# Optimization experiments

Measured on AMD Instinct MI355X. Metric: run time of the kernel, lower is better.

## Reference

```python
import jax, jax.numpy as jnp
import numpy as np

N_NODES = 50000
N_EDGES = 800000
D = 128
NEG_SLOPE = 0.2
L2_EPS = 1e-12  # torch F.normalize eps


def setup_inputs() -> dict:
    key = jax.random.key(0)
    k1, k2, k3, k4, k5 = jax.random.split(key, 5)
    node_fts = jax.random.normal(k1, (N_NODES, D), dtype=jnp.float32)
    edges = jax.random.randint(k2, (2, N_EDGES), 0, N_NODES, dtype=jnp.int32)
    edge_fts = jax.random.normal(k3, (N_EDGES, 1), dtype=jnp.float32)
    # xavier-ish init for linear weights (stored as [out, in], matching nn.Linear)
    scale = 1.414 * np.sqrt(2.0 / (D + D))
    W_self = jax.random.normal(k4, (D, D), dtype=jnp.float32) * scale
    W_neigh = jax.random.normal(k5, (D, D), dtype=jnp.float32) * scale
    return {"node_fts": node_fts, "edges": edges, "edge_fts": edge_fts,
            "W_self": W_self, "W_neigh": W_neigh}


def reference(node_fts, edges, edge_fts, W_self, W_neigh):
    n = node_fts.shape[0]
    dst_idx = edges[0]  # segment ids (aggregation targets)
    src_idx = edges[1]  # gather ids (neighbor features)

    # self transform: [N, D]
    src_node_fts = node_fts @ W_self.T

    # gather neighbor feats along edges: [E, D]
    gathered = node_fts[src_idx]

    # scatter-mean into destination nodes
    seg_sum = jax.ops.segment_sum(gathered, dst_idx, num_segments=n)  # [N, D]
    cnt = jax.ops.segment_sum(jnp.ones((gathered.shape[0], 1), dtype=node_fts.dtype),
                              dst_idx, num_segments=n)                # [N, 1]
    neigh_mean = seg_sum / jnp.maximum(cnt, 1.0)

    # linear + LeakyReLU(0.2) on aggregated neighbors
    neigh_final = jax.nn.leaky_relu(neigh_mean @ W_neigh.T, NEG_SLOPE)

    # update: sum + LeakyReLU(0.2)
    updated = jax.nn.leaky_relu(src_node_fts + neigh_final, NEG_SLOPE)

    # L2 normalize per row (torch F.normalize semantics)
    norm = jnp.linalg.norm(updated, axis=1, keepdims=True)
    return updated / jnp.maximum(norm, L2_EPS)
```

## Files before the change

### kernel.cpp

```cpp
#include <hip/hip_runtime.h>
#include <hip/hip_bf16.h>

#define N_NODES 50000
#define N_EDGES 800000
#define D 128
#define NEG 0.2f

#define NB 200
#define EPB 4000
#define NPAIR 12500
#define NCH 8
#define ROWS_PER_CH 25

#define MFMA_BLOCKS 782
#define COLA_BLOCKS 391
#define FILL_SLICES 1600
#define FILL_EPS 500

typedef __attribute__((ext_vector_type(8))) short bf16x8;
typedef __attribute__((ext_vector_type(4))) float f32x4;

__device__ __forceinline__ float bflo(unsigned int u) {
    return __uint_as_float(u << 16);
}
__device__ __forceinline__ float bfhi(unsigned int u) {
    return __uint_as_float(u & 0xffff0000u);
}

__global__ __launch_bounds__(256) void hist_convert_kernel(
    const int* __restrict__ dst_idx,
    unsigned int* __restrict__ bh,
    unsigned char* __restrict__ rank8,
    const float4* __restrict__ ws4, const float4* __restrict__ wn4,
    ushort4* __restrict__ wb4) {
    __shared__ unsigned int lh[NPAIR];
    const int tid = threadIdx.x, b = blockIdx.x;
    if (b < NB) {
        for (int i = tid; i < NPAIR; i += 256) lh[i] = 0u;
        __syncthreads();
        const int e0 = b * EPB;
        for (int i = tid; i < EPB; i += 256) {
            int d = dst_idx[e0 + i];
            int sh = (d & 3) * 8;
            unsigned int old = atomicAdd(&lh[d >> 2], 1u << sh);
            rank8[e0 + i] = (unsigned char)((old >> sh) & 0xffu);
        }
        __syncthreads();
        for (int i = tid; i < NPAIR; i += 256) bh[(size_t)b * NPAIR + i] = lh[i];
    } else {
        int i = (b - NB) * 256 + tid;
        const int NW = D * D / 4;
        if (i < 2 * NW) {
            float4 v = (i < NW) ? ws4[i] : wn4[i - NW];
            ushort4 o;
            __hip_bfloat16 h;
            h = __float2bfloat16(v.x); o.x = reinterpret_cast<unsigned short&>(h);
            h = __float2bfloat16(v.y); o.y = reinterpret_cast<unsigned short&>(h);
            h = __float2bfloat16(v.z); o.z = reinterpret_cast<unsigned short&>(h);
            h = __float2bfloat16(v.w); o.w = reinterpret_cast<unsigned short&>(h);
            wb4[i] = o;
        }
    }
}

__global__ __launch_bounds__(256) void mfma_colA_kernel(
    const float* __restrict__ x, const ushort* __restrict__ wb,
    unsigned int* __restrict__ sb32, unsigned int* __restrict__ zb32,
    const unsigned int* __restrict__ bh, unsigned int* __restrict__ csum) {
    __shared__ ushort tile[4][2][16][132];
    if (blockIdx.x < MFMA_BLOCKS) {
        const int lane = threadIdx.x & 63;
        const int wv = threadIdx.x >> 6;
        const int wglobal = blockIdx.x * 4 + wv;
        if (wglobal >= N_NODES / 16) return;
        const int m0 = wglobal * 16;
        const int lm = lane & 15;
        const int lk = (lane >> 4) * 8;

        bf16x8 a[4];
#pragma unroll
        for (int kc = 0; kc < 4; ++kc) {
            const float* src = x + (long)(m0 + lm) * D + kc * 32 + lk;
            float4 f0 = *(const float4*)(src);
            float4 f1 = *(const float4*)(src + 4);
            bf16x8 af;
            __hip_bfloat16 h;
            h = __float2bfloat16(f0.x); af[0] = reinterpret_cast<short&>(h);
            h = __float2bfloat16(f0.y); af[1] = reinterpret_cast<short&>(h);
            h = __float2bfloat16(f0.z); af[2] = reinterpret_cast<short&>(h);
            h = __float2bfloat16(f0.w); af[3] = reinterpret_cast<short&>(h);
            h = __float2bfloat16(f1.x); af[4] = reinterpret_cast<short&>(h);
            h = __float2bfloat16(f1.y); af[5] = reinterpret_cast<short&>(h);
            h = __float2bfloat16(f1.z); af[6] = reinterpret_cast<short&>(h);
            h = __float2bfloat16(f1.w); af[7] = reinterpret_cast<short&>(h);
            a[kc] = af;
        }

        const int dr = (lane >> 4) * 4;
        ushort (*ts)[132] = tile[wv][0];
        ushort (*tz)[132] = tile[wv][1];
#pragma unroll
        for (int nt = 0; nt < 16; ++nt) {
            f32x4 acc = {0.f, 0.f, 0.f, 0.f};
#pragma unroll
            for (int kc = 0; kc < 4; ++kc) {
                bf16x8 bfr = *(const bf16x8*)(wb + (nt * 16 + lm) * D + kc * 32 + lk);
                acc = __builtin_amdgcn_mfma_f32_16x16x32_bf16(a[kc], bfr, acc, 0, 0, 0);
            }
            ushort (*t)[132] = (nt < 8) ? ts : tz;
            const int col = (nt & 7) * 16 + lm;
#pragma unroll
            for (int r = 0; r < 4; ++r) {
                __hip_bfloat16 h = __float2bfloat16(acc[r]);
                t[dr + r][col] = reinterpret_cast<unsigned short&>(h);
            }
        }
        const unsigned int* ts32 = (const unsigned int*)ts;
        const unsigned int* tz32 = (const unsigned int*)tz;
#pragma unroll
        for (int r16 = 0; r16 < 16; ++r16) {
            sb32[(m0 + r16) * 64 + lane] = ts32[r16 * 66 + lane];
            zb32[(m0 + r16) * 64 + lane] = tz32[r16 * 66 + lane];
        }
    } else {
        int gid = (blockIdx.x - MFMA_BLOCKS) * 256 + threadIdx.x;
        if (gid >= NCH * NPAIR) return;
        int c = gid / NPAIR;
        int i = gid - c * NPAIR;
        const unsigned int* col = bh + (size_t)(c * ROWS_PER_CH) * NPAIR + i;
        unsigned int s = 0u;
#pragma unroll
        for (int r = 0; r < ROWS_PER_CH; ++r) s += col[(size_t)r * NPAIR];
        csum[c * NPAIR + i] = s;
    }
}

__global__ __launch_bounds__(1024) void colscanb_scan_kernel(
    unsigned int* __restrict__ bh, const unsigned int* __restrict__ csum,
    int* __restrict__ offs) {
    const int tid = threadIdx.x;
    if (blockIdx.x < 98) {
        int gid = blockIdx.x * 1024 + tid;
        if (gid >= NCH * NPAIR) return;
        int c = gid / NPAIR;
        int i = gid - c * NPAIR;
        unsigned int run = 0u;
        for (int cc = 0; cc < c; ++cc) run += csum[cc * NPAIR + i];
        unsigned int* col = bh + (size_t)(c * ROWS_PER_CH) * NPAIR + i;
#pragma unroll
        for (int r = 0; r < ROWS_PER_CH; ++r) {
            unsigned int v = col[(size_t)r * NPAIR];
            col[(size_t)r * NPAIR] = run;
            run += v;
        }
        return;
    }
    __shared__ int wsum[16];
    __shared__ int carry_s;
    const int lane = tid & 63, wv = tid >> 6;
    if (tid == 0) { carry_s = 0; offs[N_NODES] = N_EDGES; }
    __syncthreads();
    for (int base = 0; base < NPAIR; base += 4096) {
        int i0 = base + tid * 4;
        unsigned int p0 = 0, p1 = 0, p2 = 0, p3 = 0;
#pragma unroll
        for (int j = 0; j < 4; ++j) {
            int qi = i0 + j;
            if (qi < NPAIR) {
                unsigned int s = 0;
#pragma unroll
                for (int c = 0; c < NCH; ++c) s += csum[c * NPAIR + qi];
                if (j == 0) p0 = s; else if (j == 1) p1 = s;
                else if (j == 2) p2 = s; else p3 = s;
            }
        }
        int q0 = (int)((p0 & 0xffu) + ((p0 >> 8) & 0xffu) + ((p0 >> 16) & 0xffu) + (p0 >> 24));
        int q1 = (int)((p1 & 0xffu) + ((p1 >> 8) & 0xffu) + ((p1 >> 16) & 0xffu) + (p1 >> 24));
        int q2 = (int)((p2 & 0xffu) + ((p2 >> 8) & 0xffu) + ((p2 >> 16) & 0xffu) + (p2 >> 24));
        int q3 = (int)((p3 & 0xffu) + ((p3 >> 8) & 0xffu) + ((p3 >> 16) & 0xffu) + (p3 >> 24));
        int tsum = q0 + q1 + q2 + q3;
        int xs = tsum;
#pragma unroll
        for (int off = 1; off < 64; off <<= 1) {
            int y = __shfl_up(xs, off);
            if (lane >= off) xs += y;
        }
        if (lane == 63) wsum[wv] = xs;
        __syncthreads();
        if (wv == 0 && lane < 16) {
            int s = wsum[lane];
#pragma unroll
            for (int off = 1; off < 16; off <<= 1) {
                int y = __shfl_up(s, off);
                if (lane >= off) s += y;
            }
            wsum[lane] = s;
        }
        __syncthreads();
        int waveoff = (wv == 0) ? 0 : wsum[wv - 1];
        int excl = carry_s + waveoff + xs - tsum;
        unsigned int pk[4] = {p0, p1, p2, p3};
        int qs[4] = {q0, q1, q2, q3};
        int qbase = excl;
#pragma unroll
        for (int j = 0; j < 4; ++j) {
            int qi = i0 + j;
            if (qi < NPAIR) {
                unsigned int p = pk[j];
                int d0 = (int)(p & 0xffu), d1 = (int)((p >> 8) & 0xffu);
                int d2 = (int)((p >> 16) & 0xffu);
                int4 o; o.x = qbase; o.y = o.x + d0; o.z = o.y + d1; o.w = o.z + d2;
                *(int4*)(offs + 4 * qi) = o;
            }
            qbase += qs[j];
        }
        int total = wsum[15];
        __syncthreads();
        if (tid == 0) carry_s += total;
        __syncthreads();
    }
}

__global__ __launch_bounds__(256) void fill_kernel(
    const int* __restrict__ dst_idx, const int* __restrict__ src_idx,
    const unsigned char* __restrict__ rank8,
    const unsigned char* __restrict__ bprefix,
    const int* __restrict__ offs, unsigned short* __restrict__ adj) {
    const int e0 = blockIdx.x * FILL_EPS;
    const int b = e0 / EPB;
    const unsigned char* bp = bprefix + (size_t)b * N_NODES;
    for (int i = threadIdx.x; i < FILL_EPS; i += 256) {
        int e = e0 + i;
        int d = dst_idx[e];
        int pos = offs[d] + (int)bp[d] + (int)rank8[e];
        adj[pos] = (unsigned short)src_idx[e];
    }
}

__global__ __launch_bounds__(256) void gather_final_kernel(
    const uint4* __restrict__ zb4, const uint4* __restrict__ sb4,
    const int* __restrict__ offs,
    const unsigned short* __restrict__ adj, float4* __restrict__ out4) {
    int wid = (int)((blockIdx.x * (long)blockDim.x + threadIdx.x) >> 6);
    int lane = threadIdx.x & 63;
    if (wid >= N_NODES) return;
    const int c = lane & 15, g = lane >> 4;
    int base = offs[wid];
    int len = offs[wid + 1] - base;

    float a0 = 0.f, a1 = 0.f, a2 = 0.f, a3 = 0.f;
    float a4 = 0.f, a5 = 0.f, a6 = 0.f, a7 = 0.f;

    int k = 0;
    for (; k + 8 <= len; k += 8) {
        unsigned int sA = adj[base + k + g];
        unsigned int sB = adj[base + k + 4 + g];
        uint4 vA = zb4[sA * 16u + c];
        uint4 vB = zb4[sB * 16u + c];
        a0 += bflo(vA.x); a1 += bfhi(vA.x);
        a2 += bflo(vA.y); a3 += bfhi(vA.y);
        a4 += bflo(vA.z); a5 += bfhi(vA.z);
        a6 += bflo(vA.w); a7 += bfhi(vA.w);
        a0 += bflo(vB.x); a1 += bfhi(vB.x);
        a2 += bflo(vB.y); a3 += bfhi(vB.y);
        a4 += bflo(vB.z); a5 += bfhi(vB.z);
        a6 += bflo(vB.w); a7 += bfhi(vB.w);
    }
    if (k + 4 <= len) {
        unsigned int sA = adj[base + k + g];
        uint4 vA = zb4[sA * 16u + c];
        a0 += bflo(vA.x); a1 += bfhi(vA.x);
        a2 += bflo(vA.y); a3 += bfhi(vA.y);
        a4 += bflo(vA.z); a5 += bfhi(vA.z);
        a6 += bflo(vA.w); a7 += bfhi(vA.w);
        k += 4;
    }
    int rem = len - k;
    if (g < rem) {
        unsigned int sA = adj[base + k + g];
        uint4 vA = zb4[sA * 16u + c];
        a0 += bflo(vA.x); a1 += bfhi(vA.x);
        a2 += bflo(vA.y); a3 += bfhi(vA.y);
        a4 += bflo(vA.z); a5 += bfhi(vA.z);
        a6 += bflo(vA.w); a7 += bfhi(vA.w);
    }

    a0 += __shfl_xor(a0, 16); a1 += __shfl_xor(a1, 16);
    a2 += __shfl_xor(a2, 16); a3 += __shfl_xor(a3, 16);
    a4 += __shfl_xor(a4, 16); a5 += __shfl_xor(a5, 16);
    a6 += __shfl_xor(a6, 16); a7 += __shfl_xor(a7, 16);
    a0 += __shfl_xor(a0, 32); a1 += __shfl_xor(a1, 32);
    a2 += __shfl_xor(a2, 32); a3 += __shfl_xor(a3, 32);
    a4 += __shfl_xor(a4, 32); a5 += __shfl_xor(a5, 32);
    a6 += __shfl_xor(a6, 32); a7 += __shfl_xor(a7, 32);

    float inv = 1.0f / fmaxf((float)len, 1.0f);
    float m0 = a0 * inv, m1 = a1 * inv, m2 = a2 * inv, m3 = a3 * inv;
    float m4 = a4 * inv, m5 = a5 * inv, m6 = a6 * inv, m7 = a7 * inv;
    m0 = m0 > 0.f ? m0 : NEG * m0; m1 = m1 > 0.f ? m1 : NEG * m1;
    m2 = m2 > 0.f ? m2 : NEG * m2; m3 = m3 > 0.f ? m3 : NEG * m3;
    m4 = m4 > 0.f ? m4 : NEG * m4; m5 = m5 > 0.f ? m5 : NEG * m5;
    m6 = m6 > 0.f ? m6 : NEG * m6; m7 = m7 > 0.f ? m7 : NEG * m7;

    uint4 sv = sb4[(unsigned int)wid * 16u + c];
    float u0 = bflo(sv.x) + m0, u1 = bfhi(sv.x) + m1;
    float u2 = bflo(sv.y) + m2, u3 = bfhi(sv.y) + m3;
    float u4 = bflo(sv.z) + m4, u5 = bfhi(sv.z) + m5;
    float u6 = bflo(sv.w) + m6, u7 = bfhi(sv.w) + m7;
    u0 = u0 > 0.f ? u0 : NEG * u0; u1 = u1 > 0.f ? u1 : NEG * u1;
    u2 = u2 > 0.f ? u2 : NEG * u2; u3 = u3 > 0.f ? u3 : NEG * u3;
    u4 = u4 > 0.f ? u4 : NEG * u4; u5 = u5 > 0.f ? u5 : NEG * u5;
    u6 = u6 > 0.f ? u6 : NEG * u6; u7 = u7 > 0.f ? u7 : NEG * u7;

    float ss = u0 * u0 + u1 * u1 + u2 * u2 + u3 * u3 +
               u4 * u4 + u5 * u5 + u6 * u6 + u7 * u7;
    ss += __shfl_xor(ss, 1);
    ss += __shfl_xor(ss, 2);
    ss += __shfl_xor(ss, 4);
    ss += __shfl_xor(ss, 8);
    float r = 1.0f / fmaxf(sqrtf(ss), 1e-12f);

    if (lane < 16) {
        float4 o0; o0.x = u0 * r; o0.y = u1 * r; o0.z = u2 * r; o0.w = u3 * r;
        float4 o1; o1.x = u4 * r; o1.y = u5 * r; o1.z = u6 * r; o1.w = u7 * r;
        out4[(unsigned int)wid * 32u + c * 2u] = o0;
        out4[(unsigned int)wid * 32u + c * 2u + 1u] = o1;
    }
}

extern "C" void kernel_launch(void* const* d_in, const int* in_sizes, int n_in,
                              void* d_out, int out_size, void* d_ws, size_t ws_size,
                              hipStream_t stream) {
    const float* node_fts = (const float*)d_in[0];
    const int* edges = (const int*)d_in[1];
    const float* W_self = (const float*)d_in[3];
    const float* W_neigh = (const float*)d_in[4];

    const int* dst_idx = edges;
    const int* src_idx = edges + N_EDGES;

    unsigned short* zb = (unsigned short*)d_ws;
    unsigned short* sb = zb + (size_t)N_NODES * D;
    unsigned short* wb = sb + (size_t)N_NODES * D;
    int* offs = (int*)(wb + 256 * 128);
    unsigned short* adj = (unsigned short*)(offs + N_NODES + 1);
    unsigned int* bh = (unsigned int*)(adj + N_EDGES);
    unsigned char* rank8 = (unsigned char*)(bh + (size_t)NB * NPAIR);
    unsigned int* csum = (unsigned int*)(rank8 + N_EDGES);

    hist_convert_kernel<<<NB + 32, 256, 0, stream>>>(
        dst_idx, bh, rank8,
        (const float4*)W_self, (const float4*)W_neigh, (ushort4*)wb);

    mfma_colA_kernel<<<MFMA_BLOCKS + COLA_BLOCKS, 256, 0, stream>>>(
        node_fts, wb, (unsigned int*)sb, (unsigned int*)zb, bh, csum);

    colscanb_scan_kernel<<<99, 1024, 0, stream>>>(bh, csum, offs);

    fill_kernel<<<FILL_SLICES, 256, 0, stream>>>(
        dst_idx, src_idx, rank8, (const unsigned char*)bh, offs, adj);

    int gb = (N_NODES * 64 + 255) / 256;
    gather_final_kernel<<<gb, 256, 0, stream>>>(
        (const uint4*)zb, (const uint4*)sb, offs, adj, (float4*)d_out);
}
```

Baseline: 122.3 us.

## Replace per-block histogram CSR build with global atomic count and atomic fill

Replaces the blocked byte-packed histogram, column sums and two-level scan with a global atomic count per destination node, a single-block scan fused into the MFMA kernel, and an atomic cursor in the fill kernel. This drops one kernel launch plus the large bh/csum traffic, but adds a memset and global atomics on 50k counters. Edge order within each adjacency list is no longer deterministic, so floating-point summation order can vary between runs. The single scan block now runs serially over 50k entries alongside the MFMA blocks.

```diff
diff --git a/kernel.cpp b/kernel.cpp
--- a/kernel.cpp
+++ b/kernel.cpp
@@ -6,16 +6,11 @@
 #define D 128
 #define NEG 0.2f
 
-#define NB 200
-#define EPB 4000
-#define NPAIR 12500
-#define NCH 8
-#define ROWS_PER_CH 25
-
+#define CNT_BLOCKS 800
+#define CNT_EPB 1000
 #define MFMA_BLOCKS 782
-#define COLA_BLOCKS 391
-#define FILL_SLICES 1600
-#define FILL_EPS 500
+#define FILL_BLOCKS 800
+#define FILL_EPS 1000
 
 typedef __attribute__((ext_vector_type(8))) short bf16x8;
 typedef __attribute__((ext_vector_type(4))) float f32x4;
@@ -27,28 +22,18 @@
     return __uint_as_float(u & 0xffff0000u);
 }
 
-__global__ __launch_bounds__(256) void hist_convert_kernel(
-    const int* __restrict__ dst_idx,
-    unsigned int* __restrict__ bh,
-    unsigned char* __restrict__ rank8,
+__global__ __launch_bounds__(256) void count_convert_kernel(
+    const int* __restrict__ dst_idx, unsigned int* __restrict__ cnt,
     const float4* __restrict__ ws4, const float4* __restrict__ wn4,
     ushort4* __restrict__ wb4) {
-    __shared__ unsigned int lh[NPAIR];
     const int tid = threadIdx.x, b = blockIdx.x;
-    if (b < NB) {
-        for (int i = tid; i < NPAIR; i += 256) lh[i] = 0u;
-        __syncthreads();
-        const int e0 = b * EPB;
-        for (int i = tid; i < EPB; i += 256) {
-            int d = dst_idx[e0 + i];
-            int sh = (d & 3) * 8;
-            unsigned int old = atomicAdd(&lh[d >> 2], 1u << sh);
-            rank8[e0 + i] = (unsigned char)((old >> sh) & 0xffu);
-        }
-        __syncthreads();
-        for (int i = tid; i < NPAIR; i += 256) bh[(size_t)b * NPAIR + i] = lh[i];
+    if (b < CNT_BLOCKS) {
+        const int e0 = b * CNT_EPB;
+        for (int i = tid; i < CNT_EPB; i += 256) {
+            atomicAdd(&cnt[dst_idx[e0 + i]], 1u);
+        }
     } else {
-        int i = (b - NB) * 256 + tid;
+        int i = (b - CNT_BLOCKS) * 256 + tid;
         const int NW = D * D / 4;
         if (i < 2 * NW) {
             float4 v = (i < NW) ? ws4[i] : wn4[i - NW];
@@ -63,15 +48,16 @@
     }
 }
 
-__global__ __launch_bounds__(256) void mfma_colA_kernel(
+__global__ __launch_bounds__(256) void mfma_scan_kernel(
     const float* __restrict__ x, const ushort* __restrict__ wb,
     unsigned int* __restrict__ sb32, unsigned int* __restrict__ zb32,
-    const unsigned int* __restrict__ bh, unsigned int* __restrict__ csum) {
+    const unsigned int* __restrict__ cnt,
+    int* __restrict__ offs, unsigned int* __restrict__ cur) {
     __shared__ ushort tile[4][2][16][132];
-    if (blockIdx.x < MFMA_BLOCKS) {
+    if (blockIdx.x != 0) {
         const int lane = threadIdx.x & 63;
         const int wv = threadIdx.x >> 6;
-        const int wglobal = blockIdx.x * 4 + wv;
+        const int wglobal = (blockIdx.x - 1) * 4 + wv;
         if (wglobal >= N_NODES / 16) return;
         const int m0 = wglobal * 16;
         const int lm = lane & 15;
@@ -123,116 +109,67 @@
             zb32[(m0 + r16) * 64 + lane] = tz32[r16 * 66 + lane];
         }
     } else {
-        int gid = (blockIdx.x - MFMA_BLOCKS) * 256 + threadIdx.x;
-        if (gid >= NCH * NPAIR) return;
-        int c = gid / NPAIR;
-        int i = gid - c * NPAIR;
-        const unsigned int* col = bh + (size_t)(c * ROWS_PER_CH) * NPAIR + i;
-        unsigned int s = 0u;
-#pragma unroll
-        for (int r = 0; r < ROWS_PER_CH; ++r) s += col[(size_t)r * NPAIR];
-        csum[c * NPAIR + i] = s;
-    }
-}
-
-__global__ __launch_bounds__(1024) void colscanb_scan_kernel(
-    unsigned int* __restrict__ bh, const unsigned int* __restrict__ csum,
-    int* __restrict__ offs) {
-    const int tid = threadIdx.x;
-    if (blockIdx.x < 98) {
-        int gid = blockIdx.x * 1024 + tid;
-        if (gid >= NCH * NPAIR) return;
-        int c = gid / NPAIR;
-        int i = gid - c * NPAIR;
-        unsigned int run = 0u;
-        for (int cc = 0; cc < c; ++cc) run += csum[cc * NPAIR + i];
-        unsigned int* col = bh + (size_t)(c * ROWS_PER_CH) * NPAIR + i;
-#pragma unroll
-        for (int r = 0; r < ROWS_PER_CH; ++r) {
-            unsigned int v = col[(size_t)r * NPAIR];
-            col[(size_t)r * NPAIR] = run;
-            run += v;
-        }
-        return;
-    }
-    __shared__ int wsum[16];
-    __shared__ int carry_s;
-    const int lane = tid & 63, wv = tid >> 6;
-    if (tid == 0) { carry_s = 0; offs[N_NODES] = N_EDGES; }
-    __syncthreads();
-    for (int base = 0; base < NPAIR; base += 4096) {
-        int i0 = base + tid * 4;
-        unsigned int p0 = 0, p1 = 0, p2 = 0, p3 = 0;
-#pragma unroll
-        for (int j = 0; j < 4; ++j) {
-            int qi = i0 + j;
-            if (qi < NPAIR) {
-                unsigned int s = 0;
-#pragma unroll
-                for (int c = 0; c < NCH; ++c) s += csum[c * NPAIR + qi];
-                if (j == 0) p0 = s; else if (j == 1) p1 = s;
-                else if (j == 2) p2 = s; else p3 = s;
-            }
-        }
-        int q0 = (int)((p0 & 0xffu) + ((p0 >> 8) & 0xffu) + ((p0 >> 16) & 0xffu) + (p0 >> 24));
-        int q1 = (int)((p1 & 0xffu) + ((p1 >> 8) & 0xffu) + ((p1 >> 16) & 0xffu) + (p1 >> 24));
-        int q2 = (int)((p2 & 0xffu) + ((p2 >> 8) & 0xffu) + ((p2 >> 16) & 0xffu) + (p2 >> 24));
-        int q3 = (int)((p3 & 0xffu) + ((p3 >> 8) & 0xffu) + ((p3 >> 16) & 0xffu) + (p3 >> 24));
-        int tsum = q0 + q1 + q2 + q3;
-        int xs = tsum;
-#pragma unroll
-        for (int off = 1; off < 64; off <<= 1) {
-            int y = __shfl_up(xs, off);
-            if (lane >= off) xs += y;
-        }
-        if (lane == 63) wsum[wv] = xs;
+        __shared__ unsigned int wsum[4];
+        __shared__ unsigned int carry_s;
+        const int tid = threadIdx.x;
+        const int lane = tid & 63, wv = tid >> 6;
+        if (tid == 0) { carry_s = 0u; offs[N_NODES] = N_EDGES; }
         __syncthreads();
-        if (wv == 0 && lane < 16) {
-            int s = wsum[lane];
-#pragma unroll
-            for (int off = 1; off < 16; off <<= 1) {
-                int y = __shfl_up(s, off);
-                if (lane >= off) s += y;
-            }
-            wsum[lane] = s;
-        }
-        __syncthreads();
-        int waveoff = (wv == 0) ? 0 : wsum[wv - 1];
-        int excl = carry_s + waveoff + xs - tsum;
-        unsigned int pk[4] = {p0, p1, p2, p3};
-        int qs[4] = {q0, q1, q2, q3};
-        int qbase = excl;
-#pragma unroll
-        for (int j = 0; j < 4; ++j) {
-            int qi = i0 + j;
-            if (qi < NPAIR) {
-                unsigned int p = pk[j];
-                int d0 = (int)(p & 0xffu), d1 = (int)((p >> 8) & 0xffu);
-                int d2 = (int)((p >> 16) & 0xffu);
-                int4 o; o.x = qbase; o.y = o.x + d0; o.z = o.y + d1; o.w = o.z + d2;
-                *(int4*)(offs + 4 * qi) = o;
-            }
-            qbase += qs[j];
-        }
-        int total = wsum[15];
-        __syncthreads();
-        if (tid == 0) carry_s += total;
-        __syncthreads();
+        for (int base = 0; base < N_NODES; base += 1024) {
+            const int i0 = base + tid * 4;
+            uint4 v; v.x = 0u; v.y = 0u; v.z = 0u; v.w = 0u;
+            if (i0 + 4 <= N_NODES) {
+                v = *(const uint4*)(cnt + i0);
+            } else if (i0 < N_NODES) {
+                v.x = cnt[i0];
+                if (i0 + 1 < N_NODES) v.y = cnt[i0 + 1];
+                if (i0 + 2 < N_NODES) v.z = cnt[i0 + 2];
+                if (i0 + 3 < N_NODES) v.w = cnt[i0 + 3];
+            }
+            int tsum = (int)(v.x + v.y + v.z + v.w);
+            int xs = tsum;
+#pragma unroll
+            for (int off = 1; off < 64; off <<= 1) {
+                int y = __shfl_up(xs, off);
+                if (lane >= off) xs += y;
+            }
+            if (lane == 63) wsum[wv] = (unsigned int)xs;
+            __syncthreads();
+            int woff = 0;
+            for (int w = 0; w < wv; ++w) woff += (int)wsum[w];
+            int excl = (int)carry_s + woff + xs - tsum;
+            if (i0 + 4 <= N_NODES) {
+                int4 o;
+                o.x = excl;
+                o.y = o.x + (int)v.x;
+                o.z = o.y + (int)v.y;
+                o.w = o.z + (int)v.z;
+                *(int4*)(offs + i0) = o;
+                *(int4*)(cur + i0) = o;
+            } else if (i0 < N_NODES) {
+                int run = excl;
+                unsigned int e0 = v.x, e1 = v.y, e2 = v.z;
+                offs[i0] = run; cur[i0] = (unsigned int)run;
+                if (i0 + 1 < N_NODES) { run += (int)e0; offs[i0 + 1] = run; cur[i0 + 1] = (unsigned int)run; }
+                if (i0 + 2 < N_NODES) { run += (int)e1; offs[i0 + 2] = run; cur[i0 + 2] = (unsigned int)run; }
+                if (i0 + 3 < N_NODES) { run += (int)e2; offs[i0 + 3] = run; cur[i0 + 3] = (unsigned int)run; }
+            }
+            int tot = (int)(wsum[0] + wsum[1] + wsum[2] + wsum[3]);
+            __syncthreads();
+            if (tid == 0) carry_s += (unsigned int)tot;
+            __syncthreads();
+        }
     }
 }
 
 __global__ __launch_bounds__(256) void fill_kernel(
     const int* __restrict__ dst_idx, const int* __restrict__ src_idx,
-    const unsigned char* __restrict__ rank8,
-    const unsigned char* __restrict__ bprefix,
-    const int* __restrict__ offs, unsigned short* __restrict__ adj) {
+    unsigned int* __restrict__ cur, unsigned short* __restrict__ adj) {
     const int e0 = blockIdx.x * FILL_EPS;
-    const int b = e0 / EPB;
-    const unsigned char* bp = bprefix + (size_t)b * N_NODES;
     for (int i = threadIdx.x; i < FILL_EPS; i += 256) {
         int e = e0 + i;
         int d = dst_idx[e];
-        int pos = offs[d] + (int)bp[d] + (int)rank8[e];
+        unsigned int pos = atomicAdd(&cur[d], 1u);
         adj[pos] = (unsigned short)src_idx[e];
     }
 }
@@ -342,23 +279,21 @@
     unsigned short* zb = (unsigned short*)d_ws;
     unsigned short* sb = zb + (size_t)N_NODES * D;
     unsigned short* wb = sb + (size_t)N_NODES * D;
-    int* offs = (int*)(wb + 256 * 128);
+    unsigned int* cnt = (unsigned int*)(wb + 256 * 128);
+    unsigned int* cur = cnt + N_NODES;
+    int* offs = (int*)(cur + N_NODES);
     unsigned short* adj = (unsigned short*)(offs + N_NODES + 1);
-    unsigned int* bh = (unsigned int*)(adj + N_EDGES);
-    unsigned char* rank8 = (unsigned char*)(bh + (size_t)NB * NPAIR);
-    unsigned int* csum = (unsigned int*)(rank8 + N_EDGES);
-
-    hist_convert_kernel<<<NB + 32, 256, 0, stream>>>(
-        dst_idx, bh, rank8,
-        (const float4*)W_self, (const float4*)W_neigh, (ushort4*)wb);
-
-    mfma_colA_kernel<<<MFMA_BLOCKS + COLA_BLOCKS, 256, 0, stream>>>(
-        node_fts, wb, (unsigned int*)sb, (unsigned int*)zb, bh, csum);
-
-    colscanb_scan_kernel<<<99, 1024, 0, stream>>>(bh, csum, offs);
-
-    fill_kernel<<<FILL_SLICES, 256, 0, stream>>>(
-        dst_idx, src_idx, rank8, (const unsigned char*)bh, offs, adj);
+
+    hipMemsetAsync(cnt, 0, N_NODES * sizeof(unsigned int), stream);
+
+    count_convert_kernel<<<CNT_BLOCKS + 32, 256, 0, stream>>>(
+        dst_idx, cnt, (const float4*)W_self, (const float4*)W_neigh,
+        (ushort4*)wb);
+
+    mfma_scan_kernel<<<MFMA_BLOCKS + 1, 256, 0, stream>>>(
+        node_fts, wb, (unsigned int*)sb, (unsigned int*)zb, cnt, offs, cur);
+
+    fill_kernel<<<FILL_BLOCKS, 256, 0, stream>>>(dst_idx, src_idx, cur, adj);
 
     int gb = (N_NODES * 64 + 255) / 256;
     gather_final_kernel<<<gb, 256, 0, stream>>>(
```

After: 191.9 us. +56.9%, slower.
